# Kernel optimization log

Measured on AMD Instinct MI355X. Metric: run time of the kernel, lower is better.

## Reference

```python
import jax, jax.numpy as jnp
import numpy as np

B_SZ, N, NX, NU, NY, NW = 128, 2048, 64, 32, 64, 64


def setup_inputs() -> dict:
    key = jax.random.key(0)
    ks = jax.random.split(key, 10)
    sx = 1.0 / np.sqrt(NX)
    su = 1.0 / np.sqrt(NU)
    sw = 1.0 / np.sqrt(NW)
    return {
        "x0": jax.random.normal(ks[0], (B_SZ, NX), jnp.float32),
        "us": jax.random.normal(ks[1], (B_SZ, N, NU), jnp.float32),
        # state matrix scaled for (approximate) stability of the recurrence
        "A": 0.9 * sx * jax.random.normal(ks[2], (NX, NX), jnp.float32),
        "B1": su * jax.random.normal(ks[3], (NX, NU), jnp.float32),
        "B2": sw * jax.random.normal(ks[4], (NX, NW), jnp.float32),
        "C1": sx * jax.random.normal(ks[5], (NY, NX), jnp.float32),
        "D11": su * jax.random.normal(ks[6], (NY, NU), jnp.float32),
        "D12": sw * jax.random.normal(ks[7], (NY, NW), jnp.float32),
        "C2": sx * jax.random.normal(ks[8], (NW, NX), jnp.float32),
        "D21": su * jax.random.normal(ks[9], (NW, NU), jnp.float32),
    }


def reference(x0, us, A, B1, B2, C1, D11, D12, C2, D21):
    """LureSystem.forward: sequential Lure recurrence with tanh nonlinearity.

    x0: [B, nx], us: [B, N, nu] -> ys: [B, N, ny]
    Per step k (matching torch: x is updated BEFORE computing y_k):
      w = tanh(C2 x + D21 u_k)
      x <- A x + B1 u_k + B2 w
      y_k = C1 x + D11 u_k + D12 w
    """
    def step(x, u):
        w = jnp.tanh(x @ C2.T + u @ D21.T)          # [B, nw]
        x_next = x @ A.T + u @ B1.T + w @ B2.T      # [B, nx]
        y = x_next @ C1.T + u @ D11.T + w @ D12.T   # [B, ny]
        return x_next, y

    us_t = jnp.swapaxes(us, 0, 1)                    # [N, B, nu]
    _, ys_t = jax.lax.scan(step, x0, us_t)           # ys_t: [N, B, ny]
    return jnp.swapaxes(ys_t, 0, 1)                  # [B, N, ny]
```

## Files before the change

### kernel.cpp

```cpp
#include <hip/hip_runtime.h>


#define NT 2048

typedef __attribute__((ext_vector_type(8))) short short8;
typedef __attribute__((ext_vector_type(4))) float f4;
typedef __attribute__((ext_vector_type(2))) int i2;

union Frag { int i[4]; short8 v; };

__device__ __forceinline__ unsigned rne_bf16(float f) {
  unsigned u = __float_as_uint(f);
  return (u + 0x7FFFu + ((u >> 16) & 1u)) >> 16;
}
__device__ __forceinline__ void split2(float a, float b, int& hi, int& lo) {
  unsigned ha = rne_bf16(a), hb = rne_bf16(b);
  float ra = a - __uint_as_float(ha << 16);
  float rb = b - __uint_as_float(hb << 16);
  hi = (int)(ha | (hb << 16));
  lo = (int)(rne_bf16(ra) | (rne_bf16(rb) << 16));
}
__device__ __forceinline__ void split8(const float* x, Frag& hi, Frag& lo) {
#pragma unroll
  for (int p = 0; p < 4; p++) split2(x[2 * p], x[2 * p + 1], hi.i[p], lo.i[p]);
}
__device__ __forceinline__ float ftanh(float x) {
  float e = __expf(2.0f * x);
  return 1.0f - 2.0f * __builtin_amdgcn_rcpf(e + 1.0f);
}
__device__ __forceinline__ f4 mf(const Frag& a, const Frag& b, f4 c) {
  return __builtin_amdgcn_mfma_f32_16x16x32_bf16(a.v, b.v, c, 0, 0, 0);
}
__device__ __forceinline__ void lds_barrier() {
  __builtin_amdgcn_s_waitcnt(0xC07F);
  __builtin_amdgcn_s_barrier();
}
__device__ __forceinline__ void wfrag(const float* W, int row0, int c, int lane,
                                      Frag& hi, Frag& lo) {
  const int m = lane & 15, qq = lane >> 4;
  const f4* p = (const f4*)(W + (size_t)(row0 + m) * 192 + 32 * c + 8 * qq);
  f4 a = p[0], b = p[1];
  float t[8] = {a[0], a[1], a[2], a[3], b[0], b[1], b[2], b[3]};
  split8(t, hi, lo);
}

__global__ void prep_w(const float* __restrict__ A, const float* __restrict__ B1,
                       const float* __restrict__ B2, const float* __restrict__ C1,
                       const float* __restrict__ D11, const float* __restrict__ D12,
                       const float* __restrict__ C2, const float* __restrict__ D21,
                       float* __restrict__ Wfull) {
  const int r = blockIdx.x;
  const int c = threadIdx.x;
  float v = 0.f;
  if (c < 64) {
    const int j = c;
    if (r < 64) v = A[r * 64 + j];
    else if (r < 128) { float s = 0.f; for (int l = 0; l < 64; l++) s += C2[(r - 64) * 64 + l] * A[l * 64 + j]; v = s; }
    else { float s = 0.f; for (int l = 0; l < 64; l++) s += C1[(r - 128) * 64 + l] * A[l * 64 + j]; v = s; }
  } else if (c < 128) {
    const int j = c - 64;
    if (r < 64) v = B2[r * 64 + j];
    else if (r < 128) { float s = 0.f; for (int l = 0; l < 64; l++) s += C2[(r - 64) * 64 + l] * B2[l * 64 + j]; v = s; }
    else { float s = 0.f; for (int l = 0; l < 64; l++) s += C1[(r - 128) * 64 + l] * B2[l * 64 + j]; v = s + D12[(r - 128) * 64 + j]; }
  } else if (c < 160) {
    const int j = c - 128;
    if (r < 64) v = B1[r * 32 + j];
    else if (r < 128) { float s = 0.f; for (int l = 0; l < 64; l++) s += C2[(r - 64) * 64 + l] * B1[l * 32 + j]; v = s; }
    else { float s = 0.f; for (int l = 0; l < 64; l++) s += C1[(r - 128) * 64 + l] * B1[l * 32 + j]; v = s + D11[(r - 128) * 32 + j]; }
  } else {
    const int j = c - 160;
    v = (r >= 64 && r < 128) ? D21[(r - 64) * 32 + j] : 0.f;
  }
  Wfull[r * 192 + c] = v;
}

__global__ __launch_bounds__(256)
void prep_uu(const float* __restrict__ us, const float* __restrict__ Wfull,
             float* __restrict__ UU) {
  const int blk = blockIdx.x;
  const int kc = blockIdx.y;
  const int wv = threadIdx.x >> 6;
  const int lane = threadIdx.x & 63;
  const int nn = lane & 15, q = lane >> 4;
  const int b0 = blk * 16;

  Frag zh4, zl4, zh5, zl5, xh4, xl4, yh4, yl4;
  wfrag(Wfull, 64 + 16 * wv, 4, lane, zh4, zl4);
  wfrag(Wfull, 64 + 16 * wv, 5, lane, zh5, zl5);
  wfrag(Wfull, 16 * wv, 4, lane, xh4, xl4);
  wfrag(Wfull, 128 + 16 * wv, 4, lane, yh4, yl4);

  const float* ubase = us + (size_t)(b0 + nn) * (NT * 32) + 8 * q;

  int k = kc * 32;
  Frag uhc, ulc, uhn, uln;
  {
    const f4* p = (const f4*)(ubase + (size_t)k * 32);
    f4 a = p[0], b = p[1];
    float t[8] = {a[0], a[1], a[2], a[3], b[0], b[1], b[2], b[3]};
    split8(t, uhc, ulc);
  }
  f4 ra, rb;
  {
    const int kn = (k + 1 < NT) ? k + 1 : NT - 1;
    const f4* p = (const f4*)(ubase + (size_t)kn * 32);
    ra = p[0]; rb = p[1];
  }
  for (int k0 = 0; k0 < 32; k0++, k++) {
    {
      float t[8] = {ra[0], ra[1], ra[2], ra[3], rb[0], rb[1], rb[2], rb[3]};
      split8(t, uhn, uln);
    }
    {
      const int kp = (k + 2 < NT) ? k + 2 : NT - 1;
      const f4* p = (const f4*)(ubase + (size_t)kp * 32);
      ra = p[0]; rb = p[1];
    }
    f4 az = {0.f, 0.f, 0.f, 0.f}, ax = az, ay = az;
    az = mf(zh4, uhc, az); az = mf(zh5, uhn, az);
    az = mf(zh4, ulc, az); az = mf(zh5, uln, az);
    az = mf(zl4, uhc, az); az = mf(zl5, uhn, az);
    ax = mf(xh4, uhc, ax); ax = mf(xh4, ulc, ax); ax = mf(xl4, uhc, ax);
    ay = mf(yh4, uhc, ay); ay = mf(yh4, ulc, ay); ay = mf(yl4, uhc, ay);
    float* dst = UU + ((size_t)k * 8 + blk) * 3072 + lane * 4;
    *(f4*)(dst + wv * 256) = az;
    *(f4*)(dst + (4 + wv) * 256) = ax;
    *(f4*)(dst + (8 + wv) * 256) = ay;
    uhc = uhn; ulc = uln;
  }
}

__global__ __launch_bounds__(512, 1)
void lure_seq8(const float* __restrict__ x0, const float* __restrict__ us,
               const float* __restrict__ C2, const float* __restrict__ D21,
               const float* __restrict__ Wfull, const float* __restrict__ UU,
               float* __restrict__ out) {
  __shared__ int lds[2][8][272];
  const int tid = threadIdx.x;
  const int wave = tid >> 6;
  const int lane = tid & 63;
  const int q = lane >> 4;
  const int nn = lane & 15;
  const int b0 = blockIdx.x * 16;
  const int ro = q * 68 + nn * 4;
  const size_t KSTRIDE = 8 * 12 * 256;

  if (tid < 256) {
    const int n = tid >> 4;
    const int f0 = (tid & 15) * 4;
    const int cc = f0 >> 5;
    const int g = (f0 & 31) >> 3;
    const int d = (f0 & 7) >> 1;
    const int idx = g * 68 + n * 4 + d;
    const float* xrow = x0 + (b0 + n) * 64;
    float xv[4] = {xrow[f0], xrow[f0 + 1], xrow[f0 + 2], xrow[f0 + 3]};
    int h0, l0, h1, l1;
    split2(xv[0], xv[1], h0, l0);
    split2(xv[2], xv[3], h1, l1);
    lds[0][cc][idx] = h0;     lds[0][cc][idx + 1] = h1;
    lds[0][2 + cc][idx] = l0; lds[0][2 + cc][idx + 1] = l1;
    float zv[4] = {0.f, 0.f, 0.f, 0.f};
    for (int j = 0; j < 64; j++) {
      float xj = xrow[j];
#pragma unroll
      for (int r = 0; r < 4; r++) zv[r] += C2[(f0 + r) * 64 + j] * xj;
    }
    const float* urow = us + (size_t)(b0 + n) * (NT * 32);
    for (int j = 0; j < 32; j++) {
      float uj = urow[j];
#pragma unroll
      for (int r = 0; r < 4; r++) zv[r] += D21[(f0 + r) * 32 + j] * uj;
    }
#pragma unroll
    for (int r = 0; r < 4; r++) zv[r] = ftanh(zv[r]);
    split2(zv[0], zv[1], h0, l0);
    split2(zv[2], zv[3], h1, l1);
    lds[0][4 + cc][idx] = h0; lds[0][4 + cc][idx + 1] = h1;
    lds[0][6 + cc][idx] = l0; lds[0][6 + cc][idx + 1] = l1;
  }

  if (wave < 4) {
    const int zt = wave;
    Frag WH[4], WL[4];
#pragma unroll
    for (int c = 0; c < 4; c++) wfrag(Wfull, 64 + 16 * zt, c, lane, WH[c], WL[c]);
    const float* up = UU + (((size_t)blockIdx.x * 12 + zt) * 64 + lane) * 4;
    f4 uz[4];
#pragma unroll
    for (int d = 0; d < 4; d++) uz[d] = *(const f4*)(up + (size_t)d * KSTRIDE);
    const int widx = (2 * (zt & 1) + (q >> 1)) * 68 + nn * 4 + 2 * (q & 1);
    const int sh = 4 + (zt >> 1), sl = 6 + (zt >> 1);
    lds_barrier();

    auto zstep = [&](int kk, int d) {
      const int rb = kk & 1;
      Frag bh[4], bl[4];
#pragma unroll
      for (int c = 0; c < 4; c++) {
        const int s = (c < 2) ? c : 2 + c;
        bh[c].v = *(const short8*)&lds[rb][s][ro];
        bl[c].v = *(const short8*)&lds[rb][s + 2][ro];
      }
      f4 s1 = uz[d];
      f4 s2 = {0.f, 0.f, 0.f, 0.f}, s3 = s2;
#pragma unroll
      for (int c = 0; c < 4; c++) {
        s1 = mf(WH[c], bh[c], s1);
        s2 = mf(WH[c], bl[c], s2);
        s3 = mf(WL[c], bh[c], s3);
      }
      const int kp = (kk + 4 < NT) ? kk + 4 : NT - 1;
      uz[d] = *(const f4*)(up + (size_t)kp * KSTRIDE);
      float wv[4];
#pragma unroll
      for (int r = 0; r < 4; r++) wv[r] = ftanh(s1[r] + s2[r] + s3[r]);
      int h0, l0, h1, l1;
      split2(wv[0], wv[1], h0, l0);
      split2(wv[2], wv[3], h1, l1);
      i2 wh; wh[0] = h0; wh[1] = h1;
      i2 wl; wl[0] = l0; wl[1] = l1;
      *(i2*)&lds[rb ^ 1][sh][widx] = wh;
      *(i2*)&lds[rb ^ 1][sl][widx] = wl;
      lds_barrier();
    };
    for (int k = 0; k < NT; k += 4) {
      zstep(k, 0); zstep(k + 1, 1); zstep(k + 2, 2); zstep(k + 3, 3);
    }
  } else {
    const int xt = wave - 4;
    Frag WXH[4], WXL[4], WYH[4];
#pragma unroll
    for (int c = 0; c < 4; c++) {
      wfrag(Wfull, 16 * xt, c, lane, WXH[c], WXL[c]);
      Frag dmy;
      wfrag(Wfull, 128 + 16 * xt, c, lane, WYH[c], dmy);
    }
    const float* upx = UU + (((size_t)blockIdx.x * 12 + 4 + xt) * 64 + lane) * 4;
    const float* upy = UU + (((size_t)blockIdx.x * 12 + 8 + xt) * 64 + lane) * 4;
    f4 ux[4], uy[4];
#pragma unroll
    for (int d = 0; d < 4; d++) {
      ux[d] = *(const f4*)(upx + (size_t)d * KSTRIDE);
      uy[d] = *(const f4*)(upy + (size_t)d * KSTRIDE);
    }
    const int widx = (2 * (xt & 1) + (q >> 1)) * 68 + nn * 4 + 2 * (q & 1);
    const int sh = (xt >> 1), sl = 2 + (xt >> 1);
    float* py0 = out + (size_t)(b0 + nn) * (NT * 64) + 16 * xt + 4 * q;
    lds_barrier();

    auto xstep = [&](int kk, int d) {
      const int rb = kk & 1;
      Frag bh[4], bl[4];
#pragma unroll
      for (int c = 0; c < 4; c++) {
        const int s = (c < 2) ? c : 2 + c;
        bh[c].v = *(const short8*)&lds[rb][s][ro];
        bl[c].v = *(const short8*)&lds[rb][s + 2][ro];
      }
      f4 s1 = ux[d], sy = uy[d];
      f4 s2 = {0.f, 0.f, 0.f, 0.f}, s3 = s2;
#pragma unroll
      for (int c = 0; c < 4; c++) {
        s1 = mf(WXH[c], bh[c], s1);
        s2 = mf(WXH[c], bl[c], s2);
        s3 = mf(WXL[c], bh[c], s3);
        sy = mf(WYH[c], bh[c], sy);
      }
      const int kp = (kk + 4 < NT) ? kk + 4 : NT - 1;
      ux[d] = *(const f4*)(upx + (size_t)kp * KSTRIDE);
      uy[d] = *(const f4*)(upy + (size_t)kp * KSTRIDE);
      float xv[4];
#pragma unroll
      for (int r = 0; r < 4; r++) xv[r] = s1[r] + s2[r] + s3[r];
      int h0, l0, h1, l1;
      split2(xv[0], xv[1], h0, l0);
      split2(xv[2], xv[3], h1, l1);
      i2 wh; wh[0] = h0; wh[1] = h1;
      i2 wl; wl[0] = l0; wl[1] = l1;
      *(i2*)&lds[rb ^ 1][sh][widx] = wh;
      *(i2*)&lds[rb ^ 1][sl][widx] = wl;
      *(f4*)(py0 + (size_t)kk * 64) = sy;
      lds_barrier();
    };
    for (int k = 0; k < NT; k += 4) {
      xstep(k, 0); xstep(k + 1, 1); xstep(k + 2, 2); xstep(k + 3, 3);
    }
  }
}

__global__ __launch_bounds__(256, 1)
void lure_seq_fb(const float* __restrict__ x0, const float* __restrict__ us,
                 const float* __restrict__ C2, const float* __restrict__ D21,
                 const float* __restrict__ Wfull, float* __restrict__ out) {
  __shared__ int lds[2][8][272];
  const int tid = threadIdx.x;
  const int wave = tid >> 6;
  const int lane = tid & 63;
  const int q = lane >> 4;
  const int nn = lane & 15;
  const int b0 = blockIdx.x * 16;
  const int ro = q * 68 + nn * 4;
  {
    const int n = tid >> 4;
    const int f0 = (tid & 15) * 4;
    const int cc = f0 >> 5;
    const int g = (f0 & 31) >> 3;
    const int d = (f0 & 7) >> 1;
    const int idx = g * 68 + n * 4 + d;
    const float* xrow = x0 + (b0 + n) * 64;
    float xv[4] = {xrow[f0], xrow[f0 + 1], xrow[f0 + 2], xrow[f0 + 3]};
    int h0, l0, h1, l1;
    split2(xv[0], xv[1], h0, l0);
    split2(xv[2], xv[3], h1, l1);
    lds[0][cc][idx] = h0;     lds[0][cc][idx + 1] = h1;
    lds[0][2 + cc][idx] = l0; lds[0][2 + cc][idx + 1] = l1;
    float zv[4] = {0.f, 0.f, 0.f, 0.f};
    for (int j = 0; j < 64; j++) {
      float xj = xrow[j];
#pragma unroll
      for (int r = 0; r < 4; r++) zv[r] += C2[(f0 + r) * 64 + j] * xj;
    }
    const float* urow = us + (size_t)(b0 + n) * (NT * 32);
    for (int j = 0; j < 32; j++) {
      float uj = urow[j];
#pragma unroll
      for (int r = 0; r < 4; r++) zv[r] += D21[(f0 + r) * 32 + j] * uj;
    }
#pragma unroll
    for (int r = 0; r < 4; r++) zv[r] = ftanh(zv[r]);
    split2(zv[0], zv[1], h0, l0);
    split2(zv[2], zv[3], h1, l1);
    lds[0][4 + cc][idx] = h0; lds[0][4 + cc][idx + 1] = h1;
    lds[0][6 + cc][idx] = l0; lds[0][6 + cc][idx + 1] = l1;
  }
  Frag uh[2], ul[2];
  f4 ra0[4], ra1[4];
  const float* pu = us + ((size_t)(b0 + nn) * NT) * 32 + 8 * q;
#pragma unroll
  for (int j = 0; j < 2; j++) {
    const f4* p = (const f4*)(pu + j * 32);
    f4 a = p[0], b = p[1];
    float t[8] = {a[0], a[1], a[2], a[3], b[0], b[1], b[2], b[3]};
    split8(t, uh[j], ul[j]);
  }
#pragma unroll
  for (int j = 2; j <= 5; j++) {
    const f4* p = (const f4*)(pu + j * 32);
    ra0[j & 3] = p[0];
    ra1[j & 3] = p[1];
  }
  lds_barrier();

  if (wave < 2) {
    const int Z0 = wave * 2;
    Frag WH[2][6], WL[2][6];
#pragma unroll
    for (int t = 0; t < 2; t++)
#pragma unroll
      for (int c = 0; c < 6; c++)
        wfrag(Wfull, 64 + 16 * (Z0 + t), c, lane, WH[t][c], WL[t][c]);
    auto zstep = [&](int kk, int uu) {
      const int rb = uu & 1;
      Frag bh[4], bl[4];
#pragma unroll
      for (int c = 0; c < 4; c++) {
        const int s = (c < 2) ? c : 2 + c;
        bh[c].v = *(const short8*)&lds[rb][s][ro];
        bl[c].v = *(const short8*)&lds[rb][s + 2][ro];
      }
      const int i4 = uu & 1, i5 = (uu + 1) & 1;
#pragma unroll
      for (int t = 0; t < 2; t++) {
        f4 z4 = {0.f, 0.f, 0.f, 0.f};
        f4 s1a = z4, s1b = z4, s2a = z4, s2b = z4, s3a = z4, s3b = z4;
        s1a = mf(WH[t][0], bh[0], s1a); s1b = mf(WH[t][1], bh[1], s1b);
        s2a = mf(WH[t][0], bl[0], s2a); s2b = mf(WH[t][1], bl[1], s2b);
        s3a = mf(WL[t][0], bh[0], s3a); s3b = mf(WL[t][1], bh[1], s3b);
        s1a = mf(WH[t][2], bh[2], s1a); s1b = mf(WH[t][3], bh[3], s1b);
        s2a = mf(WH[t][2], bl[2], s2a); s2b = mf(WH[t][3], bl[3], s2b);
        s3a = mf(WL[t][2], bh[2], s3a); s3b = mf(WL[t][3], bh[3], s3b);
        s1a = mf(WH[t][4], uh[i4], s1a); s1b = mf(WH[t][5], uh[i5], s1b);
        s2a = mf(WH[t][4], ul[i4], s2a); s2b = mf(WH[t][5], ul[i5], s2b);
        s3a = mf(WL[t][4], uh[i4], s3a); s3b = mf(WL[t][5], uh[i5], s3b);
        float wv[4];
#pragma unroll
        for (int r = 0; r < 4; r++)
          wv[r] = ftanh(((s1a[r] + s1b[r]) + (s2a[r] + s2b[r])) + (s3a[r] + s3b[r]));
        int h0, l0, h1, l1;
        split2(wv[0], wv[1], h0, l0);
        split2(wv[2], wv[3], h1, l1);
        const int zt = Z0 + t;
        const int widx = (2 * (zt & 1) + (q >> 1)) * 68 + nn * 4 + 2 * (q & 1);
        i2 wh; wh[0] = h0; wh[1] = h1;
        i2 wl; wl[0] = l0; wl[1] = l1;
        *(i2*)&lds[rb ^ 1][4 + (zt >> 1)][widx] = wh;
        *(i2*)&lds[rb ^ 1][6 + (zt >> 1)][widx] = wl;
      }
      f4 a = ra0[(uu + 2) & 3], b = ra1[(uu + 2) & 3];
      float t8[8] = {a[0], a[1], a[2], a[3], b[0], b[1], b[2], b[3]};
      split8(t8, uh[uu & 1], ul[uu & 1]);
      const int kp = (kk + 6 < NT) ? kk + 6 : NT - 1;
      const f4* p = (const f4*)(pu + (size_t)kp * 32);
      ra0[(uu + 2) & 3] = p[0];
      ra1[(uu + 2) & 3] = p[1];
      lds_barrier();
    };
    for (int k = 0; k < NT; k += 4) {
      zstep(k, 0); zstep(k + 1, 1); zstep(k + 2, 2); zstep(k + 3, 3);
    }
  } else {
    const int X0 = (wave - 2) * 2;
    Frag WXH[2][5], WXL[2][5], WYH[2][5];
#pragma unroll
    for (int t = 0; t < 2; t++)
#pragma unroll
      for (int c = 0; c < 5; c++) {
        wfrag(Wfull, 16 * (X0 + t), c, lane, WXH[t][c], WXL[t][c]);
        Frag dmy;
        wfrag(Wfull, 128 + 16 * (X0 + t), c, lane, WYH[t][c], dmy);
      }
    float* py0 = out + (size_t)(b0 + nn) * (NT * 64) + 16 * X0 + 4 * q;
    auto xstep = [&](int kk, int uu) {
      const int rb = uu & 1;
      Frag bh[4], bl[4];
#pragma unroll
      for (int c = 0; c < 4; c++) {
        const int s = (c < 2) ? c : 2 + c;
        bh[c].v = *(const short8*)&lds[rb][s][ro];
        bl[c].v = *(const short8*)&lds[rb][s + 2][ro];
      }
      const int i4 = uu & 1;
#pragma unroll
      for (int t = 0; t < 2; t++) {
        f4 z4 = {0.f, 0.f, 0.f, 0.f};
        f4 s1 = z4, s2 = z4, s3 = z4, sy = z4;
#pragma unroll
        for (int c = 0; c < 4; c++) {
          s1 = mf(WXH[t][c], bh[c], s1);
          s2 = mf(WXH[t][c], bl[c], s2);
          s3 = mf(WXL[t][c], bh[c], s3);
          sy = mf(WYH[t][c], bh[c], sy);
        }
        s1 = mf(WXH[t][4], uh[i4], s1);
        s2 = mf(WXH[t][4], ul[i4], s2);
        s3 = mf(WXL[t][4], uh[i4], s3);
        sy = mf(WYH[t][4], uh[i4], sy);
        float xv[4];
#pragma unroll
        for (int r = 0; r < 4; r++) xv[r] = s1[r] + s2[r] + s3[r];
        int h0, l0, h1, l1;
        split2(xv[0], xv[1], h0, l0);
        split2(xv[2], xv[3], h1, l1);
        const int xt = X0 + t;
        const int widx = (2 * (xt & 1) + (q >> 1)) * 68 + nn * 4 + 2 * (q & 1);
        i2 wh; wh[0] = h0; wh[1] = h1;
        i2 wl; wl[0] = l0; wl[1] = l1;
        *(i2*)&lds[rb ^ 1][(xt >> 1)][widx] = wh;
        *(i2*)&lds[rb ^ 1][2 + (xt >> 1)][widx] = wl;
        *(f4*)(py0 + (size_t)kk * 64 + 16 * t) = sy;
      }
      f4 a = ra0[(uu + 2) & 3], b = ra1[(uu + 2) & 3];
      float t8[8] = {a[0], a[1], a[2], a[3], b[0], b[1], b[2], b[3]};
      split8(t8, uh[uu & 1], ul[uu & 1]);
      const int kp = (kk + 6 < NT) ? kk + 6 : NT - 1;
      const f4* p = (const f4*)(pu + (size_t)kp * 32);
      ra0[(uu + 2) & 3] = p[0];
      ra1[(uu + 2) & 3] = p[1];
      lds_barrier();
    };
    for (int k = 0; k < NT; k += 4) {
      xstep(k, 0); xstep(k + 1, 1); xstep(k + 2, 2); xstep(k + 3, 3);
    }
  }
}

extern "C" void kernel_launch(void* const* d_in, const int* in_sizes, int n_in,
                              void* d_out, int out_size, void* d_ws, size_t ws_size,
                              hipStream_t stream) {
  const float* x0  = (const float*)d_in[0];
  const float* us  = (const float*)d_in[1];
  const float* A   = (const float*)d_in[2];
  const float* B1  = (const float*)d_in[3];
  const float* B2  = (const float*)d_in[4];
  const float* C1  = (const float*)d_in[5];
  const float* D11 = (const float*)d_in[6];
  const float* D12 = (const float*)d_in[7];
  const float* C2  = (const float*)d_in[8];
  const float* D21 = (const float*)d_in[9];
  float* Wfull = (float*)d_ws;
  const size_t W_BYTES = (size_t)192 * 192 * 4;
  float* UU = (float*)((char*)d_ws + W_BYTES);
  const size_t UU_BYTES = (size_t)NT * 8 * 12 * 256 * 4;
  const bool pre = ws_size >= W_BYTES + UU_BYTES;
  float* out = (float*)d_out;

  prep_w<<<dim3(192), dim3(192), 0, stream>>>(A, B1, B2, C1, D11, D12, C2, D21, Wfull);
  if (pre) {
    prep_uu<<<dim3(8, 64), dim3(256), 0, stream>>>(us, Wfull, UU);
    lure_seq8<<<dim3(8), dim3(512), 0, stream>>>(x0, us, C2, D21, Wfull, UU, out);
  } else {
    lure_seq_fb<<<dim3(8), dim3(256), 0, stream>>>(x0, us, C2, D21, Wfull, out);
  }
}
```

Before: 1.154 ms.

## Merge z and x waves into four waves per block, add missing precomp term

The sequential kernel previously ran 8 waves per block, with 4 computing w and 4 computing x/y, synchronised every step through an LDS barrier. Now each of 4 waves computes its slice of w, x and y together. The intent is cheaper per-step barriers across fewer waves, in exchange for longer serial MFMA chains per wave and more register pressure. The prep_uu kernel also gains an extra lo*lo-style MFMA term (zl5 with uln) in the z input precompute, which changes accuracy and adds a little work.

```diff
diff --git a/kernel.cpp b/kernel.cpp
--- a/kernel.cpp
+++ b/kernel.cpp
@@ -119,7 +119,8 @@
     f4 az = {0.f, 0.f, 0.f, 0.f}, ax = az, ay = az;
     az = mf(zh4, uhc, az); az = mf(zh5, uhn, az);
     az = mf(zh4, ulc, az); az = mf(zh5, uln, az);
-    az = mf(zl4, uhc, az); az = mf(zl5, uhn, az);
+    az = mf(zl4, uhc, az); az = mf(zl5, uln, az);
+    az = mf(zl5, uhn, az);
     ax = mf(xh4, uhc, ax); ax = mf(xh4, ulc, ax); ax = mf(xl4, uhc, ax);
     ay = mf(yh4, uhc, ay); ay = mf(yh4, ulc, ay); ay = mf(yl4, uhc, ay);
     float* dst = UU + ((size_t)k * 8 + blk) * 3072 + lane * 4;
@@ -130,8 +131,8 @@
   }
 }
 
-__global__ __launch_bounds__(512, 1)
-void lure_seq8(const float* __restrict__ x0, const float* __restrict__ us,
+__global__ __launch_bounds__(256, 1)
+void lure_seq4(const float* __restrict__ x0, const float* __restrict__ us,
                const float* __restrict__ C2, const float* __restrict__ D21,
                const float* __restrict__ Wfull, const float* __restrict__ UU,
                float* __restrict__ out) {
@@ -145,7 +146,7 @@
   const int ro = q * 68 + nn * 4;
   const size_t KSTRIDE = 8 * 12 * 256;
 
-  if (tid < 256) {
+  {
     const int n = tid >> 4;
     const int f0 = (tid & 15) * 4;
     const int cc = f0 >> 5;
@@ -179,112 +180,81 @@
     lds[0][6 + cc][idx] = l0; lds[0][6 + cc][idx + 1] = l1;
   }
 
-  if (wave < 4) {
-    const int zt = wave;
-    Frag WH[4], WL[4];
-#pragma unroll
-    for (int c = 0; c < 4; c++) wfrag(Wfull, 64 + 16 * zt, c, lane, WH[c], WL[c]);
-    const float* up = UU + (((size_t)blockIdx.x * 12 + zt) * 64 + lane) * 4;
-    f4 uz[4];
-#pragma unroll
-    for (int d = 0; d < 4; d++) uz[d] = *(const f4*)(up + (size_t)d * KSTRIDE);
-    const int widx = (2 * (zt & 1) + (q >> 1)) * 68 + nn * 4 + 2 * (q & 1);
-    const int sh = 4 + (zt >> 1), sl = 6 + (zt >> 1);
+  const int t = wave;
+  Frag ZH[4], ZL[4], XH[4], XL[4], YH[4];
+#pragma unroll
+  for (int c = 0; c < 4; c++) {
+    wfrag(Wfull, 64 + 16 * t, c, lane, ZH[c], ZL[c]);
+    wfrag(Wfull, 16 * t, c, lane, XH[c], XL[c]);
+    Frag dmy;
+    wfrag(Wfull, 128 + 16 * t, c, lane, YH[c], dmy);
+  }
+  const float* upz = UU + (((size_t)blockIdx.x * 12 + t) * 64 + lane) * 4;
+  const float* upx = UU + (((size_t)blockIdx.x * 12 + 4 + t) * 64 + lane) * 4;
+  const float* upy = UU + (((size_t)blockIdx.x * 12 + 8 + t) * 64 + lane) * 4;
+  f4 uz[4], ux[4], uy[4];
+#pragma unroll
+  for (int d = 0; d < 4; d++) {
+    uz[d] = *(const f4*)(upz + (size_t)d * KSTRIDE);
+    ux[d] = *(const f4*)(upx + (size_t)d * KSTRIDE);
+    uy[d] = *(const f4*)(upy + (size_t)d * KSTRIDE);
+  }
+  const int widx = (2 * (t & 1) + (q >> 1)) * 68 + nn * 4 + 2 * (q & 1);
+  const int shw = 4 + (t >> 1), slw = 6 + (t >> 1);
+  const int shx = (t >> 1), slx = 2 + (t >> 1);
+  float* py0 = out + (size_t)(b0 + nn) * (NT * 64) + 16 * t + 4 * q;
+  lds_barrier();
+
+  auto step = [&](int kk, int d) {
+    const int rb = kk & 1;
+    Frag bh[4], bl[4];
+#pragma unroll
+    for (int c = 0; c < 4; c++) {
+      const int s = (c < 2) ? c : 2 + c;
+      bh[c].v = *(const short8*)&lds[rb][s][ro];
+      bl[c].v = *(const short8*)&lds[rb][s + 2][ro];
+    }
+    f4 zz = {0.f, 0.f, 0.f, 0.f};
+    f4 s1 = uz[d], s2 = zz, s3 = zz;
+    f4 t1 = ux[d], t2 = zz, t3 = zz;
+    f4 sy = uy[d];
+#pragma unroll
+    for (int c = 0; c < 4; c++) {
+      s1 = mf(ZH[c], bh[c], s1);
+      s2 = mf(ZH[c], bl[c], s2);
+      s3 = mf(ZL[c], bh[c], s3);
+      t1 = mf(XH[c], bh[c], t1);
+      t2 = mf(XH[c], bl[c], t2);
+      t3 = mf(XL[c], bh[c], t3);
+      sy = mf(YH[c], bh[c], sy);
+    }
+    const int kp = (kk + 4 < NT) ? kk + 4 : NT - 1;
+    uz[d] = *(const f4*)(upz + (size_t)kp * KSTRIDE);
+    ux[d] = *(const f4*)(upx + (size_t)kp * KSTRIDE);
+    uy[d] = *(const f4*)(upy + (size_t)kp * KSTRIDE);
+    float wv[4], xv[4];
+#pragma unroll
+    for (int r = 0; r < 4; r++) wv[r] = ftanh(s1[r] + s2[r] + s3[r]);
+#pragma unroll
+    for (int r = 0; r < 4; r++) xv[r] = t1[r] + t2[r] + t3[r];
+    int h0, l0, h1, l1;
+    split2(wv[0], wv[1], h0, l0);
+    split2(wv[2], wv[3], h1, l1);
+    i2 wh; wh[0] = h0; wh[1] = h1;
+    i2 wl; wl[0] = l0; wl[1] = l1;
+    *(i2*)&lds[rb ^ 1][shw][widx] = wh;
+    *(i2*)&lds[rb ^ 1][slw][widx] = wl;
+    split2(xv[0], xv[1], h0, l0);
+    split2(xv[2], xv[3], h1, l1);
+    i2 xh; xh[0] = h0; xh[1] = h1;
+    i2 xl; xl[0] = l0; xl[1] = l1;
+    *(i2*)&lds[rb ^ 1][shx][widx] = xh;
+    *(i2*)&lds[rb ^ 1][slx][widx] = xl;
+    *(f4*)(py0 + (size_t)kk * 64) = sy;
     lds_barrier();
-
-    auto zstep = [&](int kk, int d) {
-      const int rb = kk & 1;
-      Frag bh[4], bl[4];
-#pragma unroll
-      for (int c = 0; c < 4; c++) {
-        const int s = (c < 2) ? c : 2 + c;
-        bh[c].v = *(const short8*)&lds[rb][s][ro];
-        bl[c].v = *(const short8*)&lds[rb][s + 2][ro];
-      }
-      f4 s1 = uz[d];
-      f4 s2 = {0.f, 0.f, 0.f, 0.f}, s3 = s2;
-#pragma unroll
-      for (int c = 0; c < 4; c++) {
-        s1 = mf(WH[c], bh[c], s1);
-        s2 = mf(WH[c], bl[c], s2);
-        s3 = mf(WL[c], bh[c], s3);
-      }
-      const int kp = (kk + 4 < NT) ? kk + 4 : NT - 1;
-      uz[d] = *(const f4*)(up + (size_t)kp * KSTRIDE);
-      float wv[4];
-#pragma unroll
-      for (int r = 0; r < 4; r++) wv[r] = ftanh(s1[r] + s2[r] + s3[r]);
-      int h0, l0, h1, l1;
-      split2(wv[0], wv[1], h0, l0);
-      split2(wv[2], wv[3], h1, l1);
-      i2 wh; wh[0] = h0; wh[1] = h1;
-      i2 wl; wl[0] = l0; wl[1] = l1;
-      *(i2*)&lds[rb ^ 1][sh][widx] = wh;
-      *(i2*)&lds[rb ^ 1][sl][widx] = wl;
-      lds_barrier();
-    };
-    for (int k = 0; k < NT; k += 4) {
-      zstep(k, 0); zstep(k + 1, 1); zstep(k + 2, 2); zstep(k + 3, 3);
-    }
-  } else {
-    const int xt = wave - 4;
-    Frag WXH[4], WXL[4], WYH[4];
-#pragma unroll
-    for (int c = 0; c < 4; c++) {
-      wfrag(Wfull, 16 * xt, c, lane, WXH[c], WXL[c]);
-      Frag dmy;
-      wfrag(Wfull, 128 + 16 * xt, c, lane, WYH[c], dmy);
-    }
-    const float* upx = UU + (((size_t)blockIdx.x * 12 + 4 + xt) * 64 + lane) * 4;
-    const float* upy = UU + (((size_t)blockIdx.x * 12 + 8 + xt) * 64 + lane) * 4;
-    f4 ux[4], uy[4];
-#pragma unroll
-    for (int d = 0; d < 4; d++) {
-      ux[d] = *(const f4*)(upx + (size_t)d * KSTRIDE);
-      uy[d] = *(const f4*)(upy + (size_t)d * KSTRIDE);
-    }
-    const int widx = (2 * (xt & 1) + (q >> 1)) * 68 + nn * 4 + 2 * (q & 1);
-    const int sh = (xt >> 1), sl = 2 + (xt >> 1);
-    float* py0 = out + (size_t)(b0 + nn) * (NT * 64) + 16 * xt + 4 * q;
-    lds_barrier();
-
-    auto xstep = [&](int kk, int d) {
-      const int rb = kk & 1;
-      Frag bh[4], bl[4];
-#pragma unroll
-      for (int c = 0; c < 4; c++) {
-        const int s = (c < 2) ? c : 2 + c;
-        bh[c].v = *(const short8*)&lds[rb][s][ro];
-        bl[c].v = *(const short8*)&lds[rb][s + 2][ro];
-      }
-      f4 s1 = ux[d], sy = uy[d];
-      f4 s2 = {0.f, 0.f, 0.f, 0.f}, s3 = s2;
-#pragma unroll
-      for (int c = 0; c < 4; c++) {
-        s1 = mf(WXH[c], bh[c], s1);
-        s2 = mf(WXH[c], bl[c], s2);
-        s3 = mf(WXL[c], bh[c], s3);
-        sy = mf(WYH[c], bh[c], sy);
-      }
-      const int kp = (kk + 4 < NT) ? kk + 4 : NT - 1;
-      ux[d] = *(const f4*)(upx + (size_t)kp * KSTRIDE);
-      uy[d] = *(const f4*)(upy + (size_t)kp * KSTRIDE);
-      float xv[4];
-#pragma unroll
-      for (int r = 0; r < 4; r++) xv[r] = s1[r] + s2[r] + s3[r];
-      int h0, l0, h1, l1;
-      split2(xv[0], xv[1], h0, l0);
-      split2(xv[2], xv[3], h1, l1);
-      i2 wh; wh[0] = h0; wh[1] = h1;
-      i2 wl; wl[0] = l0; wl[1] = l1;
-      *(i2*)&lds[rb ^ 1][sh][widx] = wh;
-      *(i2*)&lds[rb ^ 1][sl][widx] = wl;
-      *(f4*)(py0 + (size_t)kk * 64) = sy;
-      lds_barrier();
-    };
-    for (int k = 0; k < NT; k += 4) {
-      xstep(k, 0); xstep(k + 1, 1); xstep(k + 2, 2); xstep(k + 3, 3);
-    }
+  };
+  for (int k = 0; k < NT; k += 4) {
+    step(k, 0); step(k + 1, 1); step(k + 2, 2); step(k + 3, 3);
   }
 }
 
@@ -497,7 +467,7 @@
   prep_w<<<dim3(192), dim3(192), 0, stream>>>(A, B1, B2, C1, D11, D12, C2, D21, Wfull);
   if (pre) {
     prep_uu<<<dim3(8, 64), dim3(256), 0, stream>>>(us, Wfull, UU);
-    lure_seq8<<<dim3(8), dim3(512), 0, stream>>>(x0, us, C2, D21, Wfull, UU, out);
+    lure_seq4<<<dim3(8), dim3(256), 0, stream>>>(x0, us, C2, D21, Wfull, UU, out);
   } else {
     lure_seq_fb<<<dim3(8), dim3(256), 0, stream>>>(x0, us, C2, D21, Wfull, out);
   }
```

New measurement: 1.428 ms. 23.8% more time.

## Pack hi/lo bf16 halves into one MFMA K-dim and split batch across 16 blocks

Applied to the files above, without the earlier changes.

Each workgroup now handles 8 batch rows instead of 16, and the grid doubles to 16 blocks. The hi and lo bf16 parts of the state go into the two halves of the 16-column MFMA B operand, and a DPP row-rotate folds the two column halves back together. This cuts the MFMAs per step from 3 (or 4) to 2 (or 3) and halves the LDS fragment reads, which shortens the serial per-step latency chain. The cost is half the MFMA columns wasted on duplicate work, masked lanes, and extra DPP adds.

```diff
diff --git a/kernel.cpp b/kernel.cpp
--- a/kernel.cpp
+++ b/kernel.cpp
@@ -7,7 +7,7 @@
 typedef __attribute__((ext_vector_type(4))) float f4;
 typedef __attribute__((ext_vector_type(2))) int i2;
 
-union Frag { int i[4]; short8 v; };
+union Frag { int i[4]; i2 h[2]; short8 v; };
 
 __device__ __forceinline__ unsigned rne_bf16(float f) {
   unsigned u = __float_as_uint(f);
@@ -30,6 +30,10 @@
 }
 __device__ __forceinline__ f4 mf(const Frag& a, const Frag& b, f4 c) {
   return __builtin_amdgcn_mfma_f32_16x16x32_bf16(a.v, b.v, c, 0, 0, 0);
+}
+__device__ __forceinline__ float ror8f(float x) {
+  return __int_as_float(
+      __builtin_amdgcn_mov_dpp(__float_as_int(x), 0x128, 0xf, 0xf, true));
 }
 __device__ __forceinline__ void lds_barrier() {
   __builtin_amdgcn_s_waitcnt(0xC07F);
@@ -131,41 +135,44 @@
 }
 
 __global__ __launch_bounds__(512, 1)
-void lure_seq8(const float* __restrict__ x0, const float* __restrict__ us,
+void lure_seqp(const float* __restrict__ x0, const float* __restrict__ us,
                const float* __restrict__ C2, const float* __restrict__ D21,
                const float* __restrict__ Wfull, const float* __restrict__ UU,
                float* __restrict__ out) {
-  __shared__ int lds[2][8][272];
+  __shared__ int lds[2][4][272];
   const int tid = threadIdx.x;
   const int wave = tid >> 6;
   const int lane = tid & 63;
   const int q = lane >> 4;
   const int nn = lane & 15;
-  const int b0 = blockIdx.x * 16;
+  const int b8 = blockIdx.x * 8;
   const int ro = q * 68 + nn * 4;
   const size_t KSTRIDE = 8 * 12 * 256;
-
-  if (tid < 256) {
+  const int ob = blockIdx.x >> 1, hh = blockIdx.x & 1;
+  const int ulane = 8 * hh + (lane & 7) + 16 * q;
+  const float msk = (lane & 8) ? 0.f : 1.f;
+
+  if (tid < 128) {
     const int n = tid >> 4;
     const int f0 = (tid & 15) * 4;
-    const int cc = f0 >> 5;
+    const int c = f0 >> 5;
     const int g = (f0 & 31) >> 3;
     const int d = (f0 & 7) >> 1;
     const int idx = g * 68 + n * 4 + d;
-    const float* xrow = x0 + (b0 + n) * 64;
+    const float* xrow = x0 + (b8 + n) * 64;
     float xv[4] = {xrow[f0], xrow[f0 + 1], xrow[f0 + 2], xrow[f0 + 3]};
     int h0, l0, h1, l1;
     split2(xv[0], xv[1], h0, l0);
     split2(xv[2], xv[3], h1, l1);
-    lds[0][cc][idx] = h0;     lds[0][cc][idx + 1] = h1;
-    lds[0][2 + cc][idx] = l0; lds[0][2 + cc][idx + 1] = l1;
+    lds[0][c][idx] = h0;       lds[0][c][idx + 1] = h1;
+    lds[0][c][idx + 32] = l0;  lds[0][c][idx + 33] = l1;
     float zv[4] = {0.f, 0.f, 0.f, 0.f};
     for (int j = 0; j < 64; j++) {
       float xj = xrow[j];
 #pragma unroll
       for (int r = 0; r < 4; r++) zv[r] += C2[(f0 + r) * 64 + j] * xj;
     }
-    const float* urow = us + (size_t)(b0 + n) * (NT * 32);
+    const float* urow = us + (size_t)(b8 + n) * (NT * 32);
     for (int j = 0; j < 32; j++) {
       float uj = urow[j];
 #pragma unroll
@@ -175,8 +182,8 @@
     for (int r = 0; r < 4; r++) zv[r] = ftanh(zv[r]);
     split2(zv[0], zv[1], h0, l0);
     split2(zv[2], zv[3], h1, l1);
-    lds[0][4 + cc][idx] = h0; lds[0][4 + cc][idx + 1] = h1;
-    lds[0][6 + cc][idx] = l0; lds[0][6 + cc][idx + 1] = l1;
+    lds[0][2 + c][idx] = h0;       lds[0][2 + c][idx + 1] = h1;
+    lds[0][2 + c][idx + 32] = l0;  lds[0][2 + c][idx + 33] = l1;
   }
 
   if (wave < 4) {
@@ -184,43 +191,40 @@
     Frag WH[4], WL[4];
 #pragma unroll
     for (int c = 0; c < 4; c++) wfrag(Wfull, 64 + 16 * zt, c, lane, WH[c], WL[c]);
-    const float* up = UU + (((size_t)blockIdx.x * 12 + zt) * 64 + lane) * 4;
+    const float* up = UU + (((size_t)ob * 12 + zt) * 64 + ulane) * 4;
     f4 uz[4];
 #pragma unroll
     for (int d = 0; d < 4; d++) uz[d] = *(const f4*)(up + (size_t)d * KSTRIDE);
     const int widx = (2 * (zt & 1) + (q >> 1)) * 68 + nn * 4 + 2 * (q & 1);
-    const int sh = 4 + (zt >> 1), sl = 6 + (zt >> 1);
+    const int rw = 2 + (zt >> 1);
     lds_barrier();
 
     auto zstep = [&](int kk, int d) {
       const int rb = kk & 1;
-      Frag bh[4], bl[4];
+      Frag b[4];
+#pragma unroll
+      for (int c = 0; c < 4; c++) b[c].v = *(const short8*)&lds[rb][c][ro];
+      f4 sA = {uz[d][0] * msk, uz[d][1] * msk, uz[d][2] * msk, uz[d][3] * msk};
+      f4 sB = {0.f, 0.f, 0.f, 0.f};
 #pragma unroll
       for (int c = 0; c < 4; c++) {
-        const int s = (c < 2) ? c : 2 + c;
-        bh[c].v = *(const short8*)&lds[rb][s][ro];
-        bl[c].v = *(const short8*)&lds[rb][s + 2][ro];
-      }
-      f4 s1 = uz[d];
-      f4 s2 = {0.f, 0.f, 0.f, 0.f}, s3 = s2;
-#pragma unroll
-      for (int c = 0; c < 4; c++) {
-        s1 = mf(WH[c], bh[c], s1);
-        s2 = mf(WH[c], bl[c], s2);
-        s3 = mf(WL[c], bh[c], s3);
+        sA = mf(WH[c], b[c], sA);
+        sB = mf(WL[c], b[c], sB);
       }
       const int kp = (kk + 4 < NT) ? kk + 4 : NT - 1;
       uz[d] = *(const f4*)(up + (size_t)kp * KSTRIDE);
       float wv[4];
 #pragma unroll
-      for (int r = 0; r < 4; r++) wv[r] = ftanh(s1[r] + s2[r] + s3[r]);
+      for (int r = 0; r < 4; r++) wv[r] = ftanh(sA[r] + ror8f(sA[r]) + sB[r]);
       int h0, l0, h1, l1;
       split2(wv[0], wv[1], h0, l0);
       split2(wv[2], wv[3], h1, l1);
-      i2 wh; wh[0] = h0; wh[1] = h1;
-      i2 wl; wl[0] = l0; wl[1] = l1;
-      *(i2*)&lds[rb ^ 1][sh][widx] = wh;
-      *(i2*)&lds[rb ^ 1][sl][widx] = wl;
+      if ((lane & 8) == 0) {
+        i2 wh; wh[0] = h0; wh[1] = h1;
+        i2 wl; wl[0] = l0; wl[1] = l1;
+        *(i2*)&lds[rb ^ 1][rw][widx] = wh;
+        *(i2*)&lds[rb ^ 1][rw][widx + 32] = wl;
+      }
       lds_barrier();
     };
     for (int k = 0; k < NT; k += 4) {
@@ -235,8 +239,8 @@
       Frag dmy;
       wfrag(Wfull, 128 + 16 * xt, c, lane, WYH[c], dmy);
     }
-    const float* upx = UU + (((size_t)blockIdx.x * 12 + 4 + xt) * 64 + lane) * 4;
-    const float* upy = UU + (((size_t)blockIdx.x * 12 + 8 + xt) * 64 + lane) * 4;
+    const float* upx = UU + (((size_t)ob * 12 + 4 + xt) * 64 + ulane) * 4;
+    const float* upy = UU + (((size_t)ob * 12 + 8 + xt) * 64 + ulane) * 4;
     f4 ux[4], uy[4];
 #pragma unroll
     for (int d = 0; d < 4; d++) {
@@ -244,42 +248,40 @@
       uy[d] = *(const f4*)(upy + (size_t)d * KSTRIDE);
     }
     const int widx = (2 * (xt & 1) + (q >> 1)) * 68 + nn * 4 + 2 * (q & 1);
-    const int sh = (xt >> 1), sl = 2 + (xt >> 1);
-    float* py0 = out + (size_t)(b0 + nn) * (NT * 64) + 16 * xt + 4 * q;
+    const int rw = (xt >> 1);
+    float* py0 = out + (size_t)(b8 + nn) * (NT * 64) + 16 * xt + 4 * q;
     lds_barrier();
 
     auto xstep = [&](int kk, int d) {
       const int rb = kk & 1;
-      Frag bh[4], bl[4];
+      Frag b[4];
+#pragma unroll
+      for (int c = 0; c < 4; c++) b[c].v = *(const short8*)&lds[rb][c][ro];
+      f4 tA = {ux[d][0] * msk, ux[d][1] * msk, ux[d][2] * msk, ux[d][3] * msk};
+      f4 tB = {0.f, 0.f, 0.f, 0.f};
+      f4 sy = uy[d];
 #pragma unroll
       for (int c = 0; c < 4; c++) {
-        const int s = (c < 2) ? c : 2 + c;
-        bh[c].v = *(const short8*)&lds[rb][s][ro];
-        bl[c].v = *(const short8*)&lds[rb][s + 2][ro];
-      }
-      f4 s1 = ux[d], sy = uy[d];
-      f4 s2 = {0.f, 0.f, 0.f, 0.f}, s3 = s2;
-#pragma unroll
-      for (int c = 0; c < 4; c++) {
-        s1 = mf(WXH[c], bh[c], s1);
-        s2 = mf(WXH[c], bl[c], s2);
-        s3 = mf(WXL[c], bh[c], s3);
-        sy = mf(WYH[c], bh[c], sy);
+        tA = mf(WXH[c], b[c], tA);
+        tB = mf(WXL[c], b[c], tB);
+        sy = mf(WYH[c], b[c], sy);
       }
       const int kp = (kk + 4 < NT) ? kk + 4 : NT - 1;
       ux[d] = *(const f4*)(upx + (size_t)kp * KSTRIDE);
       uy[d] = *(const f4*)(upy + (size_t)kp * KSTRIDE);
       float xv[4];
 #pragma unroll
-      for (int r = 0; r < 4; r++) xv[r] = s1[r] + s2[r] + s3[r];
+      for (int r = 0; r < 4; r++) xv[r] = tA[r] + ror8f(tA[r]) + tB[r];
       int h0, l0, h1, l1;
       split2(xv[0], xv[1], h0, l0);
       split2(xv[2], xv[3], h1, l1);
-      i2 wh; wh[0] = h0; wh[1] = h1;
-      i2 wl; wl[0] = l0; wl[1] = l1;
-      *(i2*)&lds[rb ^ 1][sh][widx] = wh;
-      *(i2*)&lds[rb ^ 1][sl][widx] = wl;
-      *(f4*)(py0 + (size_t)kk * 64) = sy;
+      if ((lane & 8) == 0) {
+        i2 wh; wh[0] = h0; wh[1] = h1;
+        i2 wl; wl[0] = l0; wl[1] = l1;
+        *(i2*)&lds[rb ^ 1][rw][widx] = wh;
+        *(i2*)&lds[rb ^ 1][rw][widx + 32] = wl;
+        *(f4*)(py0 + (size_t)kk * 64) = sy;
+      }
       lds_barrier();
     };
     for (int k = 0; k < NT; k += 4) {
@@ -497,7 +499,7 @@
   prep_w<<<dim3(192), dim3(192), 0, stream>>>(A, B1, B2, C1, D11, D12, C2, D21, Wfull);
   if (pre) {
     prep_uu<<<dim3(8, 64), dim3(256), 0, stream>>>(us, Wfull, UU);
-    lure_seq8<<<dim3(8), dim3(512), 0, stream>>>(x0, us, C2, D21, Wfull, UU, out);
+    lure_seqp<<<dim3(16), dim3(512), 0, stream>>>(x0, us, C2, D21, Wfull, UU, out);
   } else {
     lure_seq_fb<<<dim3(8), dim3(256), 0, stream>>>(x0, us, C2, D21, Wfull, out);
   }
```

New measurement: 1.005 ms. -12.9%, faster.
